# Optimization experiments

Hardware: AMD Instinct MI355X
Metric: run time of the kernel (lower is better)

Reference implementation:

```python
import jax, jax.numpy as jnp
import numpy as np

BINS = 256

def setup_inputs() -> dict:
    key = jax.random.key(0)
    x = jax.random.normal(key, (64, 3, 512, 512), dtype=jnp.float32)
    return {"x": x}

def reference(x):
    bins = BINS

    def equalize_one(img):
        # img: (C, H, W) -- flattened wholesale, matching the torch per-index loop
        flat = img.reshape(-1)
        mn = flat.min()
        mx = flat.max()
        norm = (flat - mn) * (bins - 1) / (mx - mn + 1e-8)
        norm = jnp.clip(norm, 0, bins - 1)
        idx = norm.astype(jnp.int32)  # bucket index per pixel
        hist = jnp.zeros((bins,), jnp.float32).at[idx].add(1.0)  # bincount
        cdf = jnp.cumsum(hist)
        cdf_norm = (cdf - cdf.min()) / (cdf.max() - cdf.min() + 1e-8)
        return cdf_norm[idx].reshape(img.shape)  # gather equalized values

    return jax.vmap(equalize_one)(x)
```

## Files before the change

### kernel.cpp

```cpp
#include <hip/hip_runtime.h>

#define NUM_BINS 256
#define NPI (3*512*512)
#define TPB 256
#define MM_BLOCKS 16
#define NSUB 16
#define SUBSTRIDE 257
#define G_VEC 4

__device__ __forceinline__ unsigned fmap(float f) {
  unsigned u = __float_as_uint(f);
  return (u & 0x80000000u) ? ~u : (u | 0x80000000u);
}
__device__ __forceinline__ float funmap(unsigned m) {
  unsigned u = (m & 0x80000000u) ? (m ^ 0x80000000u) : ~m;
  return __uint_as_float(u);
}

__device__ __forceinline__ int bin_of(float v, float mn, float denom) {
  float norm = (v - mn) * 255.0f / denom;
  norm = fminf(fmaxf(norm, 0.0f), 255.0f);
  return (int)norm;
}

__global__ void init_ws(unsigned* __restrict__ minmax, int* __restrict__ hist) {
  int b = blockIdx.x;
  hist[b * NUM_BINS + threadIdx.x] = 0;
  if (threadIdx.x == 0) { minmax[2*b] = 0xFFFFFFFFu; minmax[2*b+1] = 0u; }
}

__global__ void minmax_k(const float4* __restrict__ x, unsigned* __restrict__ minmax) {
  const int chunk4 = NPI / 4 / MM_BLOCKS;
  int img = blockIdx.x / MM_BLOCKS;
  int blk = blockIdx.x % MM_BLOCKS;
  const float4* p = x + (size_t)img * (NPI/4) + (size_t)blk * chunk4;
  float mn = 3.4e38f, mx = -3.4e38f;
  for (int i = threadIdx.x; i < chunk4; i += TPB) {
    float4 v = p[i];
    mn = fminf(mn, fminf(fminf(v.x, v.y), fminf(v.z, v.w)));
    mx = fmaxf(mx, fmaxf(fmaxf(v.x, v.y), fmaxf(v.z, v.w)));
  }
  for (int off = 32; off > 0; off >>= 1) {
    mn = fminf(mn, __shfl_down(mn, off));
    mx = fmaxf(mx, __shfl_down(mx, off));
  }
  __shared__ float smn[4], smx[4];
  int wave = threadIdx.x >> 6, lane = threadIdx.x & 63;
  if (lane == 0) { smn[wave] = mn; smx[wave] = mx; }
  __syncthreads();
  if (threadIdx.x == 0) {
    mn = fminf(fminf(smn[0], smn[1]), fminf(smn[2], smn[3]));
    mx = fmaxf(fmaxf(smx[0], smx[1]), fmaxf(smx[2], smx[3]));
    atomicMin(&minmax[2*img],   fmap(mn));
    atomicMax(&minmax[2*img+1], fmap(mx));
  }
}

__global__ void hist_k(const float4* __restrict__ x,
                       const unsigned* __restrict__ minmax,
                       int* __restrict__ hist) {
  __shared__ int sh[NSUB * SUBSTRIDE];
  for (int i = threadIdx.x; i < NSUB * SUBSTRIDE; i += TPB) sh[i] = 0;
  const int chunk4 = NPI / 4 / MM_BLOCKS;
  int img = blockIdx.x / MM_BLOCKS;
  int blk = blockIdx.x % MM_BLOCKS;
  float mn = funmap(minmax[2*img]);
  float mx = funmap(minmax[2*img+1]);
  float denom = mx - mn + 1e-8f;
  __syncthreads();
  const float4* p = x + (size_t)img * (NPI/4) + (size_t)blk * chunk4;
  int* mysub = sh + (threadIdx.x % NSUB) * SUBSTRIDE;
  for (int i = threadIdx.x; i < chunk4; i += TPB * 4) {
    float4 v0 = p[i];
    float4 v1 = p[i + TPB];
    float4 v2 = p[i + 2*TPB];
    float4 v3 = p[i + 3*TPB];
    atomicAdd(&mysub[bin_of(v0.x, mn, denom)], 1);
    atomicAdd(&mysub[bin_of(v0.y, mn, denom)], 1);
    atomicAdd(&mysub[bin_of(v0.z, mn, denom)], 1);
    atomicAdd(&mysub[bin_of(v0.w, mn, denom)], 1);
    atomicAdd(&mysub[bin_of(v1.x, mn, denom)], 1);
    atomicAdd(&mysub[bin_of(v1.y, mn, denom)], 1);
    atomicAdd(&mysub[bin_of(v1.z, mn, denom)], 1);
    atomicAdd(&mysub[bin_of(v1.w, mn, denom)], 1);
    atomicAdd(&mysub[bin_of(v2.x, mn, denom)], 1);
    atomicAdd(&mysub[bin_of(v2.y, mn, denom)], 1);
    atomicAdd(&mysub[bin_of(v2.z, mn, denom)], 1);
    atomicAdd(&mysub[bin_of(v2.w, mn, denom)], 1);
    atomicAdd(&mysub[bin_of(v3.x, mn, denom)], 1);
    atomicAdd(&mysub[bin_of(v3.y, mn, denom)], 1);
    atomicAdd(&mysub[bin_of(v3.z, mn, denom)], 1);
    atomicAdd(&mysub[bin_of(v3.w, mn, denom)], 1);
  }
  __syncthreads();
  int bin = threadIdx.x;
  int s = 0;
  #pragma unroll
  for (int c = 0; c < NSUB; ++c) s += sh[c * SUBSTRIDE + bin];
  atomicAdd(&hist[img * NUM_BINS + bin], s);
}

__global__ void scan_k(const int* __restrict__ hist, float* __restrict__ cdfn) {
  __shared__ int s[NUM_BINS];
  int img = blockIdx.x, t = threadIdx.x;
  s[t] = hist[img * NUM_BINS + t];
  __syncthreads();
  for (int off = 1; off < NUM_BINS; off <<= 1) {
    int add = (t >= off) ? s[t - off] : 0;
    __syncthreads();
    s[t] += add;
    __syncthreads();
  }
  int cdf = s[t], c0 = s[0], cN = s[NUM_BINS - 1];
  cdfn[img * NUM_BINS + t] = (float)(cdf - c0) / ((float)(cN - c0) + 1e-8f);
}

__global__ void gather_k(const float4* __restrict__ x,
                         const unsigned* __restrict__ minmax,
                         const float* __restrict__ cdfn,
                         float4* __restrict__ out) {
  __shared__ float c[NUM_BINS];
  const int f4pi = NPI / 4;
  const int CHUNK = TPB * G_VEC;
  const int bpi = f4pi / CHUNK;
  int img = blockIdx.x / bpi;
  int blk = blockIdx.x % bpi;
  c[threadIdx.x] = cdfn[img * NUM_BINS + threadIdx.x];
  float mn = funmap(minmax[2*img]);
  float denom = funmap(minmax[2*img+1]) - mn + 1e-8f;
  __syncthreads();
  size_t base = (size_t)img * f4pi + (size_t)blk * CHUNK + threadIdx.x;
  #pragma unroll
  for (int j = 0; j < G_VEC; ++j) {
    float4 v = x[base + (size_t)j * TPB];
    float4 o;
    o.x = c[bin_of(v.x, mn, denom)];
    o.y = c[bin_of(v.y, mn, denom)];
    o.z = c[bin_of(v.z, mn, denom)];
    o.w = c[bin_of(v.w, mn, denom)];
    out[base + (size_t)j * TPB] = o;
  }
}

extern "C" void kernel_launch(void* const* d_in, const int* in_sizes, int n_in,
                              void* d_out, int out_size, void* d_ws, size_t ws_size,
                              hipStream_t stream) {
  const float* x = (const float*)d_in[0];
  float* out = (float*)d_out;
  int B = in_sizes[0] / NPI;

  unsigned* minmax = (unsigned*)d_ws;
  int* hist  = (int*)((char*)d_ws + (size_t)2 * B * sizeof(unsigned));
  float* cdfn = (float*)((char*)d_ws + (size_t)2 * B * sizeof(unsigned)
                                      + (size_t)B * NUM_BINS * sizeof(int));

  init_ws<<<B, NUM_BINS, 0, stream>>>(minmax, hist);
  minmax_k<<<B * MM_BLOCKS, TPB, 0, stream>>>((const float4*)x, minmax);
  hist_k<<<B * MM_BLOCKS, TPB, 0, stream>>>((const float4*)x, minmax, hist);
  scan_k<<<B, NUM_BINS, 0, stream>>>(hist, cdfn);
  gather_k<<<B * (NPI/4/(TPB*G_VEC)), TPB, 0, stream>>>((const float4*)x, minmax, cdfn, (float4*)out);
}
```

Before: 401.0 us.

## Cache packed 8-bit bin indices in histogram pass and gather from them

```diff
diff --git a/kernel.cpp b/kernel.cpp
--- a/kernel.cpp
+++ b/kernel.cpp
@@ -4,18 +4,9 @@
 #define NPI (3*512*512)
 #define TPB 256
 #define MM_BLOCKS 16
-#define NSUB 16
+#define NSUB 32
 #define SUBSTRIDE 257
-#define G_VEC 4
-
-__device__ __forceinline__ unsigned fmap(float f) {
-  unsigned u = __float_as_uint(f);
-  return (u & 0x80000000u) ? ~u : (u | 0x80000000u);
-}
-__device__ __forceinline__ float funmap(unsigned m) {
-  unsigned u = (m & 0x80000000u) ? (m ^ 0x80000000u) : ~m;
-  return __uint_as_float(u);
-}
+#define G_VEC 8
 
 __device__ __forceinline__ int bin_of(float v, float mn, float denom) {
   float norm = (v - mn) * 255.0f / denom;
@@ -23,13 +14,12 @@
   return (int)norm;
 }
 
-__global__ void init_ws(unsigned* __restrict__ minmax, int* __restrict__ hist) {
-  int b = blockIdx.x;
-  hist[b * NUM_BINS + threadIdx.x] = 0;
-  if (threadIdx.x == 0) { minmax[2*b] = 0xFFFFFFFFu; minmax[2*b+1] = 0u; }
-}
-
-__global__ void minmax_k(const float4* __restrict__ x, unsigned* __restrict__ minmax) {
+__device__ __forceinline__ unsigned pack4(int b0, int b1, int b2, int b3) {
+  return (unsigned)b0 | ((unsigned)b1 << 8) | ((unsigned)b2 << 16) | ((unsigned)b3 << 24);
+}
+
+__global__ void minmax_k(const float4* __restrict__ x,
+                         float* __restrict__ mmn, float* __restrict__ mmx) {
   const int chunk4 = NPI / 4 / MM_BLOCKS;
   int img = blockIdx.x / MM_BLOCKS;
   int blk = blockIdx.x % MM_BLOCKS;
@@ -49,61 +39,79 @@
   if (lane == 0) { smn[wave] = mn; smx[wave] = mx; }
   __syncthreads();
   if (threadIdx.x == 0) {
-    mn = fminf(fminf(smn[0], smn[1]), fminf(smn[2], smn[3]));
-    mx = fmaxf(fmaxf(smx[0], smx[1]), fmaxf(smx[2], smx[3]));
-    atomicMin(&minmax[2*img],   fmap(mn));
-    atomicMax(&minmax[2*img+1], fmap(mx));
+    mmn[blockIdx.x] = fminf(fminf(smn[0], smn[1]), fminf(smn[2], smn[3]));
+    mmx[blockIdx.x] = fmaxf(fmaxf(smx[0], smx[1]), fmaxf(smx[2], smx[3]));
   }
 }
 
 __global__ void hist_k(const float4* __restrict__ x,
-                       const unsigned* __restrict__ minmax,
-                       int* __restrict__ hist) {
+                       const float* __restrict__ mmn, const float* __restrict__ mmx,
+                       int* __restrict__ histblk, unsigned* __restrict__ bins32) {
   __shared__ int sh[NSUB * SUBSTRIDE];
+  __shared__ float s_mn, s_dn;
   for (int i = threadIdx.x; i < NSUB * SUBSTRIDE; i += TPB) sh[i] = 0;
   const int chunk4 = NPI / 4 / MM_BLOCKS;
   int img = blockIdx.x / MM_BLOCKS;
   int blk = blockIdx.x % MM_BLOCKS;
-  float mn = funmap(minmax[2*img]);
-  float mx = funmap(minmax[2*img+1]);
-  float denom = mx - mn + 1e-8f;
-  __syncthreads();
-  const float4* p = x + (size_t)img * (NPI/4) + (size_t)blk * chunk4;
-  int* mysub = sh + (threadIdx.x % NSUB) * SUBSTRIDE;
+  if (threadIdx.x < MM_BLOCKS) {
+    float a = mmn[img * MM_BLOCKS + threadIdx.x];
+    float b = mmx[img * MM_BLOCKS + threadIdx.x];
+    for (int off = 8; off > 0; off >>= 1) {
+      a = fminf(a, __shfl_down(a, off));
+      b = fmaxf(b, __shfl_down(b, off));
+    }
+    if (threadIdx.x == 0) { s_mn = a; s_dn = b - a + 1e-8f; }
+  }
+  __syncthreads();
+  float mn = s_mn, denom = s_dn;
+  size_t gbase = (size_t)img * (NPI/4) + (size_t)blk * chunk4;
+  const float4* p = x + gbase;
+  int* mysub = sh + (threadIdx.x & (NSUB - 1)) * SUBSTRIDE;
+  bool wb = (bins32 != nullptr);
   for (int i = threadIdx.x; i < chunk4; i += TPB * 4) {
     float4 v0 = p[i];
     float4 v1 = p[i + TPB];
     float4 v2 = p[i + 2*TPB];
     float4 v3 = p[i + 3*TPB];
-    atomicAdd(&mysub[bin_of(v0.x, mn, denom)], 1);
-    atomicAdd(&mysub[bin_of(v0.y, mn, denom)], 1);
-    atomicAdd(&mysub[bin_of(v0.z, mn, denom)], 1);
-    atomicAdd(&mysub[bin_of(v0.w, mn, denom)], 1);
-    atomicAdd(&mysub[bin_of(v1.x, mn, denom)], 1);
-    atomicAdd(&mysub[bin_of(v1.y, mn, denom)], 1);
-    atomicAdd(&mysub[bin_of(v1.z, mn, denom)], 1);
-    atomicAdd(&mysub[bin_of(v1.w, mn, denom)], 1);
-    atomicAdd(&mysub[bin_of(v2.x, mn, denom)], 1);
-    atomicAdd(&mysub[bin_of(v2.y, mn, denom)], 1);
-    atomicAdd(&mysub[bin_of(v2.z, mn, denom)], 1);
-    atomicAdd(&mysub[bin_of(v2.w, mn, denom)], 1);
-    atomicAdd(&mysub[bin_of(v3.x, mn, denom)], 1);
-    atomicAdd(&mysub[bin_of(v3.y, mn, denom)], 1);
-    atomicAdd(&mysub[bin_of(v3.z, mn, denom)], 1);
-    atomicAdd(&mysub[bin_of(v3.w, mn, denom)], 1);
+    int b00 = bin_of(v0.x, mn, denom), b01 = bin_of(v0.y, mn, denom);
+    int b02 = bin_of(v0.z, mn, denom), b03 = bin_of(v0.w, mn, denom);
+    int b10 = bin_of(v1.x, mn, denom), b11 = bin_of(v1.y, mn, denom);
+    int b12 = bin_of(v1.z, mn, denom), b13 = bin_of(v1.w, mn, denom);
+    int b20 = bin_of(v2.x, mn, denom), b21 = bin_of(v2.y, mn, denom);
+    int b22 = bin_of(v2.z, mn, denom), b23 = bin_of(v2.w, mn, denom);
+    int b30 = bin_of(v3.x, mn, denom), b31 = bin_of(v3.y, mn, denom);
+    int b32 = bin_of(v3.z, mn, denom), b33 = bin_of(v3.w, mn, denom);
+    atomicAdd(&mysub[b00], 1); atomicAdd(&mysub[b01], 1);
+    atomicAdd(&mysub[b02], 1); atomicAdd(&mysub[b03], 1);
+    atomicAdd(&mysub[b10], 1); atomicAdd(&mysub[b11], 1);
+    atomicAdd(&mysub[b12], 1); atomicAdd(&mysub[b13], 1);
+    atomicAdd(&mysub[b20], 1); atomicAdd(&mysub[b21], 1);
+    atomicAdd(&mysub[b22], 1); atomicAdd(&mysub[b23], 1);
+    atomicAdd(&mysub[b30], 1); atomicAdd(&mysub[b31], 1);
+    atomicAdd(&mysub[b32], 1); atomicAdd(&mysub[b33], 1);
+    if (wb) {
+      bins32[gbase + i]           = pack4(b00, b01, b02, b03);
+      bins32[gbase + i + TPB]     = pack4(b10, b11, b12, b13);
+      bins32[gbase + i + 2*TPB]   = pack4(b20, b21, b22, b23);
+      bins32[gbase + i + 3*TPB]   = pack4(b30, b31, b32, b33);
+    }
   }
   __syncthreads();
   int bin = threadIdx.x;
   int s = 0;
   #pragma unroll
   for (int c = 0; c < NSUB; ++c) s += sh[c * SUBSTRIDE + bin];
-  atomicAdd(&hist[img * NUM_BINS + bin], s);
-}
-
-__global__ void scan_k(const int* __restrict__ hist, float* __restrict__ cdfn) {
+  histblk[blockIdx.x * NUM_BINS + bin] = s;
+}
+
+__global__ void scan_k(const int* __restrict__ histblk, float* __restrict__ cdfn) {
   __shared__ int s[NUM_BINS];
   int img = blockIdx.x, t = threadIdx.x;
-  s[t] = hist[img * NUM_BINS + t];
+  int v = 0;
+  #pragma unroll
+  for (int b = 0; b < MM_BLOCKS; ++b)
+    v += histblk[(img * MM_BLOCKS + b) * NUM_BINS + t];
+  s[t] = v;
   __syncthreads();
   for (int off = 1; off < NUM_BINS; off <<= 1) {
     int add = (t >= off) ? s[t - off] : 0;
@@ -115,10 +123,9 @@
   cdfn[img * NUM_BINS + t] = (float)(cdf - c0) / ((float)(cN - c0) + 1e-8f);
 }
 
-__global__ void gather_k(const float4* __restrict__ x,
-                         const unsigned* __restrict__ minmax,
-                         const float* __restrict__ cdfn,
-                         float4* __restrict__ out) {
+__global__ void gather_bins_k(const unsigned* __restrict__ bins32,
+                              const float* __restrict__ cdfn,
+                              float4* __restrict__ out) {
   __shared__ float c[NUM_BINS];
   const int f4pi = NPI / 4;
   const int CHUNK = TPB * G_VEC;
@@ -126,12 +133,49 @@
   int img = blockIdx.x / bpi;
   int blk = blockIdx.x % bpi;
   c[threadIdx.x] = cdfn[img * NUM_BINS + threadIdx.x];
-  float mn = funmap(minmax[2*img]);
-  float denom = funmap(minmax[2*img+1]) - mn + 1e-8f;
   __syncthreads();
   size_t base = (size_t)img * f4pi + (size_t)blk * CHUNK + threadIdx.x;
+  unsigned bv[G_VEC];
+  #pragma unroll
+  for (int j = 0; j < G_VEC; ++j) bv[j] = bins32[base + (size_t)j * TPB];
   #pragma unroll
   for (int j = 0; j < G_VEC; ++j) {
+    unsigned b = bv[j];
+    float4 o;
+    o.x = c[b & 255u];
+    o.y = c[(b >> 8) & 255u];
+    o.z = c[(b >> 16) & 255u];
+    o.w = c[b >> 24];
+    out[base + (size_t)j * TPB] = o;
+  }
+}
+
+__global__ void gather_x_k(const float4* __restrict__ x,
+                           const float* __restrict__ mmn, const float* __restrict__ mmx,
+                           const float* __restrict__ cdfn,
+                           float4* __restrict__ out) {
+  __shared__ float c[NUM_BINS];
+  __shared__ float s_mn, s_dn;
+  const int f4pi = NPI / 4;
+  const int CHUNK = TPB * 4;
+  const int bpi = f4pi / CHUNK;
+  int img = blockIdx.x / bpi;
+  int blk = blockIdx.x % bpi;
+  c[threadIdx.x] = cdfn[img * NUM_BINS + threadIdx.x];
+  if (threadIdx.x < MM_BLOCKS) {
+    float a = mmn[img * MM_BLOCKS + threadIdx.x];
+    float b = mmx[img * MM_BLOCKS + threadIdx.x];
+    for (int off = 8; off > 0; off >>= 1) {
+      a = fminf(a, __shfl_down(a, off));
+      b = fmaxf(b, __shfl_down(b, off));
+    }
+    if (threadIdx.x == 0) { s_mn = a; s_dn = b - a + 1e-8f; }
+  }
+  __syncthreads();
+  float mn = s_mn, denom = s_dn;
+  size_t base = (size_t)img * f4pi + (size_t)blk * CHUNK + threadIdx.x;
+  #pragma unroll
+  for (int j = 0; j < 4; ++j) {
     float4 v = x[base + (size_t)j * TPB];
     float4 o;
     o.x = c[bin_of(v.x, mn, denom)];
@@ -149,14 +193,23 @@
   float* out = (float*)d_out;
   int B = in_sizes[0] / NPI;
 
-  unsigned* minmax = (unsigned*)d_ws;
-  int* hist  = (int*)((char*)d_ws + (size_t)2 * B * sizeof(unsigned));
-  float* cdfn = (float*)((char*)d_ws + (size_t)2 * B * sizeof(unsigned)
-                                      + (size_t)B * NUM_BINS * sizeof(int));
-
-  init_ws<<<B, NUM_BINS, 0, stream>>>(minmax, hist);
-  minmax_k<<<B * MM_BLOCKS, TPB, 0, stream>>>((const float4*)x, minmax);
-  hist_k<<<B * MM_BLOCKS, TPB, 0, stream>>>((const float4*)x, minmax, hist);
-  scan_k<<<B, NUM_BINS, 0, stream>>>(hist, cdfn);
-  gather_k<<<B * (NPI/4/(TPB*G_VEC)), TPB, 0, stream>>>((const float4*)x, minmax, cdfn, (float4*)out);
-}
+  char* ws = (char*)d_ws;
+  float* mmn = (float*)ws;
+  float* mmx = mmn + (size_t)B * MM_BLOCKS;
+  int* histblk = (int*)(mmx + (size_t)B * MM_BLOCKS);
+  float* cdfn = (float*)(histblk + (size_t)B * MM_BLOCKS * NUM_BINS);
+  unsigned* bins32 = (unsigned*)(cdfn + (size_t)B * NUM_BINS);
+  size_t need = (size_t)((char*)bins32 - ws) + (size_t)B * NPI;
+  bool use_bins = (ws_size >= need);
+
+  minmax_k<<<B * MM_BLOCKS, TPB, 0, stream>>>((const float4*)x, mmn, mmx);
+  hist_k<<<B * MM_BLOCKS, TPB, 0, stream>>>((const float4*)x, mmn, mmx, histblk,
+                                            use_bins ? bins32 : nullptr);
+  scan_k<<<B, NUM_BINS, 0, stream>>>(histblk, cdfn);
+  if (use_bins) {
+    gather_bins_k<<<B * (NPI/4/(TPB*G_VEC)), TPB, 0, stream>>>(bins32, cdfn, (float4*)out);
+  } else {
+    gather_x_k<<<B * (NPI/4/(TPB*4)), TPB, 0, stream>>>((const float4*)x, mmn, mmx, cdfn,
+                                                        (float4*)out);
+  }
+}
```

New measurement: 392.9 us. -2.0%, faster.
